# Kernel tuning notes

Measured on AMD Instinct MI355X. Metric: run time of the kernel, lower is better.

The kernel has to match this reference:

```python
import jax, jax.numpy as jnp
import numpy as np

N, F, H, E_DIM, G, NE = 20000, 128, 256, 128, 64, 320000

def _ln(x, g, b, eps=1e-5):
    m = jnp.mean(x, axis=-1, keepdims=True)
    v = jnp.mean((x - m) ** 2, axis=-1, keepdims=True)
    return (x - m) * jax.lax.rsqrt(v + eps) * g + b

def _gcn(x, src, dst, W, b, n):
    # GCNConv: h = D^{-1/2}(A+I)D^{-1/2} (x W) + b, degrees from A+I
    h = x @ W
    loop = jnp.arange(n)
    s = jnp.concatenate([src, loop])
    d = jnp.concatenate([dst, loop])
    deg = jax.ops.segment_sum(jnp.ones_like(s, dtype=h.dtype), d, num_segments=n)
    dinv = jax.lax.rsqrt(jnp.maximum(deg, 1.0))
    w_e = dinv[s] * dinv[d]  # [E+N]
    out = jax.ops.segment_sum(h[s] * w_e[:, None], d, num_segments=n)
    return out + b

def setup_inputs() -> dict:
    key = jax.random.key(0)
    ks = jax.random.split(key, 32)
    def nrm(k, shp, scale=0.05):
        return jax.random.normal(k, shp, dtype=jnp.float32) * scale
    inp = {
        'x': jax.random.normal(ks[0], (N, F), dtype=jnp.float32),
        'edge_index': jax.random.randint(ks[1], (2, NE), 0, N),
        'batch': jnp.sort(jax.random.randint(ks[2], (N,), 0, G)),
        'enc_w': nrm(ks[3], (F, H)), 'enc_b': jnp.zeros((H,), jnp.float32),
        'enc_g': jnp.ones((H,), jnp.float32), 'enc_be': jnp.zeros((H,), jnp.float32),
        'w1': nrm(ks[4], (H, H)), 'b1': jnp.zeros((H,), jnp.float32),
        'g1': jnp.ones((H,), jnp.float32), 'be1': jnp.zeros((H,), jnp.float32),
        'w2': nrm(ks[5], (H, H)), 'b2': jnp.zeros((H,), jnp.float32),
        'g2': jnp.ones((H,), jnp.float32), 'be2': jnp.zeros((H,), jnp.float32),
        'w3': nrm(ks[6], (H, H)), 'b3': jnp.zeros((H,), jnp.float32),
        'g3': jnp.ones((H,), jnp.float32), 'be3': jnp.zeros((H,), jnp.float32),
        'attn_w': nrm(ks[7], (H, 1)), 'attn_b': jnp.zeros((1,), jnp.float32),
        'pw1': nrm(ks[8], (H, H)), 'pb1': jnp.zeros((H,), jnp.float32),
        'pg': jnp.ones((H,), jnp.float32), 'pbe': jnp.zeros((H,), jnp.float32),
        'pw2': nrm(ks[9], (H, E_DIM)), 'pb2': jnp.zeros((E_DIM,), jnp.float32),
    }
    return inp

def reference(x, edge_index, batch, enc_w, enc_b, enc_g, enc_be,
              w1, b1, g1, be1, w2, b2, g2, be2, w3, b3, g3, be3,
              attn_w, attn_b, pw1, pb1, pg, pbe, pw2, pb2):
    src, dst = edge_index[0], edge_index[1]
    n = x.shape[0]
    # feature encoder (dropout = identity in eval)
    h = jax.nn.relu(_ln(x @ enc_w + enc_b, enc_g, enc_be))
    x1 = jax.nn.relu(_ln(_gcn(h, src, dst, w1, b1, n), g1, be1))
    x2 = jax.nn.relu(_ln(_gcn(x1, src, dst, w2, b2, n), g2, be2)) + x1
    x3 = jax.nn.relu(_ln(_gcn(x2, src, dst, w3, b3, n), g3, be3)) + x2
    # global softmax over the node dimension (dim=0), as in the original
    a = jnp.tanh(x3 @ attn_w + attn_b)       # [N,1]
    a = jax.nn.softmax(a, axis=0)
    pooled = jax.ops.segment_sum(x3 * a, batch, num_segments=G)  # [G,H]
    p = jax.nn.relu(_ln(pooled @ pw1 + pb1, pg, pbe))
    out = p @ pw2 + pb2                      # [G, E_DIM]
    nrm = jnp.maximum(jnp.linalg.norm(out, axis=1, keepdims=True), 1e-12)
    return out / nrm
```

## Files before the change

kernel.cpp:

```cpp
#include <hip/hip_runtime.h>
#include <hip/hip_bf16.h>

#define NN 20000
#define FF 128
#define HH 256
#define EDIM 128
#define GG 64
#define NEDGE 320000
#define PSUB 16
#define CSTRIDE 64

typedef __attribute__((ext_vector_type(4))) float f4;
typedef __attribute__((ext_vector_type(4))) float f32x4;
typedef __attribute__((ext_vector_type(8))) short bf16x8;
typedef __attribute__((ext_vector_type(4))) unsigned short u16x4;
typedef __attribute__((ext_vector_type(4))) int i32x4;

__device__ inline float wsum(float v) {
#pragma unroll
    for (int m = 32; m >= 1; m >>= 1) v += __shfl_xor(v, m, 64);
    return v;
}

__device__ inline unsigned short f2b(float f) {
    union { float f; unsigned u; } x; x.f = f;
    unsigned r = x.u + 0x7fffu + ((x.u >> 16) & 1u);
    return (unsigned short)(r >> 16);
}
__device__ inline float b2f(unsigned short u) {
    union { unsigned u; float f; } x; x.u = ((unsigned)u) << 16;
    return x.f;
}

__global__ void k_prep(const float* __restrict__ W0, const float* __restrict__ W1,
                       const float* __restrict__ W2, const float* __restrict__ W3,
                       unsigned short* __restrict__ T0, unsigned short* __restrict__ T1,
                       unsigned short* __restrict__ T2, unsigned short* __restrict__ T3,
                       int* __restrict__ cnt) {
    int b = blockIdx.x, tid = threadIdx.x;
    if (b < 20) {
        int t = b * 256 + tid;
        if (t < NN / 4) ((i32x4*)cnt)[t] = (i32x4){0, 0, 0, 0};
        return;
    }
    const float* W; unsigned short* T; int K, tt;
    if (b < 28)      { W = W0; T = T0; K = 128; tt = b - 20; }
    else if (b < 44) { W = W1; T = T1; K = 256; tt = b - 28; }
    else if (b < 60) { W = W2; T = T2; K = 256; tt = b - 44; }
    else             { W = W3; T = T3; K = 256; tt = b - 60; }
    int ktiles = K / 64;
    int kt = tt % ktiles, nt = tt / ktiles;
    int k0 = kt * 64, n0 = nt * 64;
    __shared__ unsigned short ldsT[64][65];
    int rn = (tid & 15) * 4, rk = tid >> 4;
#pragma unroll
    for (int i = 0; i < 4; i++) {
        int k = rk + 16 * i;
        f4 v = *(const f4*)(W + (size_t)(k0 + k) * 256 + n0 + rn);
#pragma unroll
        for (int j = 0; j < 4; j++) ldsT[rn + j][k] = f2b(v[j]);
    }
    __syncthreads();
    int wn = tid >> 2, kseg = (tid & 3) * 16;
#pragma unroll
    for (int q = 0; q < 4; q++) {
        u16x4 o = { ldsT[wn][kseg + q * 4 + 0], ldsT[wn][kseg + q * 4 + 1],
                    ldsT[wn][kseg + q * 4 + 2], ldsT[wn][kseg + q * 4 + 3] };
        *(u16x4*)(T + (size_t)(n0 + wn) * K + k0 + kseg + q * 4) = o;
    }
}

__global__ __launch_bounds__(256) void k_encg1(
        const float* __restrict__ X, const unsigned short* __restrict__ Wt,
        const unsigned short* __restrict__ Wt1,
        const float* __restrict__ eb, const float* __restrict__ gam,
        const float* __restrict__ bet, unsigned short* __restrict__ T1out, int M,
        const int* __restrict__ src, const int* __restrict__ dst,
        int* __restrict__ cnt, int* __restrict__ colv, int ne) {
    __shared__ unsigned short Wl[2 * 16 * 64 * 8];
    __shared__ unsigned short hs[64 * 256];
    int b = blockIdx.x, tid = threadIdx.x;
    if (b >= 313) {
        int e = (b - 313) * 256 + tid;
        if (e < ne) {
            int d = dst[e];
            int pos = atomicAdd(&cnt[d], 1);
            if (pos < CSTRIDE) colv[(size_t)d * CSTRIDE + pos] = src[e];
        }
        return;
    }
    int wave = tid >> 6, lane = tid & 63;
    int lmod = lane & 15, ldiv = lane >> 4;
    int mbase = b * 64 + wave * 16;
    int row = min(mbase + lmod, M - 1);
    f32x4 acc[16] = {};
#pragma unroll
    for (int h = 0; h < 2; h++) {
        __syncthreads();
        for (int c = tid; c < 2048; c += 256) {
            int l = c & 63, nf = (c >> 6) & 15, kss = c >> 10;
            int n = nf * 16 + (l & 15);
            int k = (h * 2 + kss) * 32 + (l >> 4) * 8;
            *(bf16x8*)(Wl + (size_t)c * 8) = *(const bf16x8*)(Wt + (size_t)n * 128 + k);
        }
        __syncthreads();
#pragma unroll
        for (int kss = 0; kss < 2; kss++) {
            int ks = h * 2 + kss;
            f4 xa = *(const f4*)(X + (size_t)row * 128 + ks * 32 + ldiv * 8);
            f4 xb2 = *(const f4*)(X + (size_t)row * 128 + ks * 32 + ldiv * 8 + 4);
            bf16x8 xf;
            xf[0] = (short)f2b(xa[0]); xf[1] = (short)f2b(xa[1]);
            xf[2] = (short)f2b(xa[2]); xf[3] = (short)f2b(xa[3]);
            xf[4] = (short)f2b(xb2[0]); xf[5] = (short)f2b(xb2[1]);
            xf[6] = (short)f2b(xb2[2]); xf[7] = (short)f2b(xb2[3]);
#pragma unroll
            for (int nf = 0; nf < 16; nf++) {
                bf16x8 wf = *(bf16x8*)(Wl + ((size_t)(kss * 16 + nf) * 64 + lane) * 8);
                acc[nf] = __builtin_amdgcn_mfma_f32_16x16x32_bf16(wf, xf, acc[nf], 0, 0, 0);
            }
        }
    }
    float vs = 0.f;
#pragma unroll
    for (int nf = 0; nf < 16; nf++) {
        f4 bb = *(const f4*)(eb + nf * 16 + ldiv * 4);
#pragma unroll
        for (int r = 0; r < 4; r++) { acc[nf][r] += bb[r]; vs += acc[nf][r]; }
    }
    vs += __shfl_xor(vs, 16, 64); vs += __shfl_xor(vs, 32, 64);
    float mean = vs * (1.0f / 256.0f);
    float ss = 0.f;
#pragma unroll
    for (int nf = 0; nf < 16; nf++) {
#pragma unroll
        for (int r = 0; r < 4; r++) { float d = acc[nf][r] - mean; ss += d * d; }
    }
    ss += __shfl_xor(ss, 16, 64); ss += __shfl_xor(ss, 32, 64);
    float rs = rsqrtf(ss * (1.0f / 256.0f) + 1e-5f);
    int r_loc = wave * 16 + lmod;
    int swz = (r_loc & 7) << 4;
#pragma unroll
    for (int nf = 0; nf < 16; nf++) {
        f4 gv = *(const f4*)(gam + nf * 16 + ldiv * 4);
        f4 bv = *(const f4*)(bet + nf * 16 + ldiv * 4);
        u16x4 o;
#pragma unroll
        for (int r = 0; r < 4; r++)
            o[r] = f2b(fmaxf((acc[nf][r] - mean) * rs * gv[r] + bv[r], 0.0f));
        int byte = ((nf * 32 + ldiv * 8) ^ swz);
        *(u16x4*)((char*)hs + (size_t)r_loc * 512 + byte) = o;
    }
    __syncthreads();
    f32x4 acc2[4][4] = {};
    const unsigned short* wb = Wt1 + (size_t)(wave * 64 + lmod) * 256 + ldiv * 8;
#pragma unroll
    for (int ks = 0; ks < 8; ks++) {
        bf16x8 wf[4], hf[4];
#pragma unroll
        for (int nf = 0; nf < 4; nf++)
            wf[nf] = *(const bf16x8*)(wb + (size_t)nf * 16 * 256 + ks * 32);
#pragma unroll
        for (int rg = 0; rg < 4; rg++) {
            int rr = rg * 16 + lmod;
            int byte = ((ks * 64 + ldiv * 16) ^ ((rr & 7) << 4));
            hf[rg] = *(const bf16x8*)((const char*)hs + (size_t)rr * 512 + byte);
        }
#pragma unroll
        for (int rg = 0; rg < 4; rg++) {
#pragma unroll
            for (int nf = 0; nf < 4; nf++) {
                acc2[rg][nf] = __builtin_amdgcn_mfma_f32_16x16x32_bf16(
                    wf[nf], hf[rg], acc2[rg][nf], 0, 0, 0);
            }
        }
    }
#pragma unroll
    for (int rg = 0; rg < 4; rg++) {
        int m = b * 64 + rg * 16 + lmod;
        if (m < M) {
#pragma unroll
            for (int nf = 0; nf < 4; nf++) {
                int n = wave * 64 + nf * 16 + ldiv * 4;
                u16x4 o = { f2b(acc2[rg][nf][0]), f2b(acc2[rg][nf][1]),
                            f2b(acc2[rg][nf][2]), f2b(acc2[rg][nf][3]) };
                *(u16x4*)(T1out + (size_t)m * 256 + n) = o;
            }
        }
    }
}

#define GEMM_NWG 628
template<int K>
__global__ __launch_bounds__(256) void bgemm(const unsigned short* __restrict__ Xb,
                                             const unsigned short* __restrict__ Wt,
                                             unsigned short* __restrict__ C, int M) {
    constexpr int KSTEPS = K / 32;
    __shared__ unsigned short Wl[KSTEPS * 4 * 64 * 8];
    int tid = threadIdx.x;
    int orig = blockIdx.y * 4 + blockIdx.x;
    int xcd = orig & 7, rest = orig >> 3;
    constexpr int q = GEMM_NWG >> 3, r = GEMM_NWG & 7;
    int wg = (xcd < r ? xcd * (q + 1) : r * (q + 1) + (xcd - r) * q) + rest;
    int m0 = wg >> 2;
    int n0 = (wg & 3) * 64;
    for (int c = tid; c < KSTEPS * 4 * 64; c += 256) {
        int lc = c & 63;
        int nf = (c >> 6) & 3;
        int ks = c >> 8;
        int n = n0 + nf * 16 + (lc & 15);
        int k = ks * 32 + (lc >> 4) * 8;
        bf16x8 v = *(const bf16x8*)(Wt + (size_t)n * K + k);
        *(bf16x8*)(Wl + (size_t)c * 8) = v;
    }
    __syncthreads();
    int wave = tid >> 6, lane = tid & 63;
    int lmod = lane & 15, ldiv = lane >> 4;
    int mbase = m0 * 128 + wave * 32;
    f32x4 acc[2][4] = {};
#pragma unroll
    for (int ks = 0; ks < KSTEPS; ks++) {
        int k0 = ks * 32 + ldiv * 8;
        bf16x8 xf[2], wf[4];
#pragma unroll
        for (int mf = 0; mf < 2; mf++) {
            int row = mbase + mf * 16 + lmod;
            row = min(row, M - 1);
            xf[mf] = *(const bf16x8*)(Xb + (size_t)row * K + k0);
        }
#pragma unroll
        for (int nf = 0; nf < 4; nf++) {
            wf[nf] = *(const bf16x8*)(Wl + ((size_t)(ks * 4 + nf) * 64 + lane) * 8);
        }
#pragma unroll
        for (int mf = 0; mf < 2; mf++) {
#pragma unroll
            for (int nf = 0; nf < 4; nf++) {
                acc[mf][nf] = __builtin_amdgcn_mfma_f32_16x16x32_bf16(
                    wf[nf], xf[mf], acc[mf][nf], 0, 0, 0);
            }
        }
    }
#pragma unroll
    for (int mf = 0; mf < 2; mf++) {
        int m = mbase + mf * 16 + lmod;
        if (m < M) {
#pragma unroll
            for (int nf = 0; nf < 4; nf++) {
                int n = n0 + nf * 16 + ldiv * 4;
                u16x4 o = { f2b(acc[mf][nf][0]), f2b(acc[mf][nf][1]),
                            f2b(acc[mf][nf][2]), f2b(acc[mf][nf][3]) };
                *(u16x4*)(C + (size_t)m * 256 + n) = o;
            }
        }
    }
}

__global__ void k_aggln(const unsigned short* __restrict__ T, const int* __restrict__ cnt,
                        const int* __restrict__ col,
                        const float* __restrict__ b, const float* __restrict__ gam,
                        const float* __restrict__ bet, const unsigned short* __restrict__ resid,
                        unsigned short* __restrict__ out,
                        const float* __restrict__ aw, const float* __restrict__ ab,
                        float* __restrict__ elog, int n) {
    int wid = (blockIdx.x * blockDim.x + threadIdx.x) >> 6;
    int lane = threadIdx.x & 63;
    if (wid >= n) return;
    int deg = min(cnt[wid], CSTRIDE);
    const int* cr = col + (size_t)wid * CSTRIDE;
    f4 a0 = {0.f,0.f,0.f,0.f}, a1 = {0.f,0.f,0.f,0.f};
    f4 a2 = {0.f,0.f,0.f,0.f}, a3 = {0.f,0.f,0.f,0.f};
    int e = 0;
    for (; e + 7 < deg; e += 8) {
        i32x4 cA = *(const i32x4*)(cr + e);
        i32x4 cB = *(const i32x4*)(cr + e + 4);
        u16x4 r0 = ((const u16x4*)(T + (size_t)cA[0] * HH))[lane];
        u16x4 r1 = ((const u16x4*)(T + (size_t)cA[1] * HH))[lane];
        u16x4 r2 = ((const u16x4*)(T + (size_t)cA[2] * HH))[lane];
        u16x4 r3 = ((const u16x4*)(T + (size_t)cA[3] * HH))[lane];
        u16x4 r4 = ((const u16x4*)(T + (size_t)cB[0] * HH))[lane];
        u16x4 r5 = ((const u16x4*)(T + (size_t)cB[1] * HH))[lane];
        u16x4 r6 = ((const u16x4*)(T + (size_t)cB[2] * HH))[lane];
        u16x4 r7 = ((const u16x4*)(T + (size_t)cB[3] * HH))[lane];
        float w0 = rsqrtf((float)(cnt[cA[0]] + 1));
        float w1 = rsqrtf((float)(cnt[cA[1]] + 1));
        float w2 = rsqrtf((float)(cnt[cA[2]] + 1));
        float w3 = rsqrtf((float)(cnt[cA[3]] + 1));
        float w4 = rsqrtf((float)(cnt[cB[0]] + 1));
        float w5 = rsqrtf((float)(cnt[cB[1]] + 1));
        float w6 = rsqrtf((float)(cnt[cB[2]] + 1));
        float w7 = rsqrtf((float)(cnt[cB[3]] + 1));
#pragma unroll
        for (int i = 0; i < 4; i++) {
            a0[i] = fmaf(w0, b2f(r0[i]), a0[i]);
            a1[i] = fmaf(w1, b2f(r1[i]), a1[i]);
            a2[i] = fmaf(w2, b2f(r2[i]), a2[i]);
            a3[i] = fmaf(w3, b2f(r3[i]), a3[i]);
            a0[i] = fmaf(w4, b2f(r4[i]), a0[i]);
            a1[i] = fmaf(w5, b2f(r5[i]), a1[i]);
            a2[i] = fmaf(w6, b2f(r6[i]), a2[i]);
            a3[i] = fmaf(w7, b2f(r7[i]), a3[i]);
        }
    }
    for (; e + 3 < deg; e += 4) {
        i32x4 c4 = *(const i32x4*)(cr + e);
        float w0 = rsqrtf((float)(cnt[c4[0]] + 1));
        float w1 = rsqrtf((float)(cnt[c4[1]] + 1));
        float w2 = rsqrtf((float)(cnt[c4[2]] + 1));
        float w3 = rsqrtf((float)(cnt[c4[3]] + 1));
        u16x4 r0 = ((const u16x4*)(T + (size_t)c4[0] * HH))[lane];
        u16x4 r1 = ((const u16x4*)(T + (size_t)c4[1] * HH))[lane];
        u16x4 r2 = ((const u16x4*)(T + (size_t)c4[2] * HH))[lane];
        u16x4 r3 = ((const u16x4*)(T + (size_t)c4[3] * HH))[lane];
#pragma unroll
        for (int i = 0; i < 4; i++) {
            a0[i] = fmaf(w0, b2f(r0[i]), a0[i]);
            a1[i] = fmaf(w1, b2f(r1[i]), a1[i]);
            a2[i] = fmaf(w2, b2f(r2[i]), a2[i]);
            a3[i] = fmaf(w3, b2f(r3[i]), a3[i]);
        }
    }
    for (; e < deg; e++) {
        int s0 = cr[e];
        float w0 = rsqrtf((float)(cnt[s0] + 1));
        u16x4 r0 = ((const u16x4*)(T + (size_t)s0 * HH))[lane];
#pragma unroll
        for (int i = 0; i < 4; i++) a0[i] = fmaf(w0, b2f(r0[i]), a0[i]);
    }
    float di = rsqrtf((float)(deg + 1));
    u16x4 sv = ((const u16x4*)(T + (size_t)wid * HH))[lane];
    f4 bb = ((const f4*)b)[lane];
    f4 v;
#pragma unroll
    for (int i = 0; i < 4; i++)
        v[i] = di * (a0[i] + a1[i] + a2[i] + a3[i]) + (di * di) * b2f(sv[i]) + bb[i];
    float s = wsum(v[0] + v[1] + v[2] + v[3]);
    float mean = s * (1.0f / HH);
    f4 d = v - mean;
    float ss = wsum(d[0] * d[0] + d[1] * d[1] + d[2] * d[2] + d[3] * d[3]);
    float rs = rsqrtf(ss * (1.0f / HH) + 1e-5f);
    f4 gv = ((const f4*)gam)[lane], bv = ((const f4*)bet)[lane];
    f4 o = d * rs * gv + bv;
#pragma unroll
    for (int i = 0; i < 4; i++) o[i] = fmaxf(o[i], 0.0f);
    if (resid != nullptr) {
        u16x4 rv = ((const u16x4*)(resid + (size_t)wid * HH))[lane];
#pragma unroll
        for (int i = 0; i < 4; i++) o[i] += b2f(rv[i]);
    }
    u16x4 ov;
#pragma unroll
    for (int i = 0; i < 4; i++) ov[i] = f2b(o[i]);
    ((u16x4*)(out + (size_t)wid * HH))[lane] = ov;
    if (elog != nullptr) {
        f4 wv = ((const f4*)aw)[lane];
        float dotv = wsum(b2f(ov[0]) * wv[0] + b2f(ov[1]) * wv[1] +
                          b2f(ov[2]) * wv[2] + b2f(ov[3]) * wv[3]);
        if (lane == 0) elog[wid] = expf(tanhf(dotv + ab[0]));
    }
}

__device__ inline int lbound(const int* __restrict__ arr, int n, int key) {
    int lo = 0, hi = n;
    while (lo < hi) {
        int mid = (lo + hi) >> 1;
        if (arr[mid] < key) lo = mid + 1; else hi = mid;
    }
    return lo;
}

__global__ __launch_bounds__(256) void k_pool(const unsigned short* __restrict__ x3,
                                              const float* __restrict__ elog,
                                              const int* __restrict__ batch,
                                              float* __restrict__ partial,
                                              float* __restrict__ esum, int n) {
    int g = blockIdx.y, s = blockIdx.x, j = threadIdx.x;
    __shared__ int slo, shi;
    if (j == 0) { slo = lbound(batch, n, g); shi = lbound(batch, n, g + 1); }
    __syncthreads();
    int lo = slo, hi = shi;
    float a0 = 0.f, a1 = 0.f;
    int i = lo + s;
    for (; i + PSUB < hi; i += 2 * PSUB) {
        a0 += elog[i] * b2f(x3[(size_t)i * HH + j]);
        a1 += elog[i + PSUB] * b2f(x3[(size_t)(i + PSUB) * HH + j]);
    }
    if (i < hi) a0 += elog[i] * b2f(x3[(size_t)i * HH + j]);
    partial[(size_t)(g * PSUB + s) * HH + j] = a0 + a1;
    if (j < 64) {
        float es = 0.f;
        for (int t = j; (size_t)lo + s + (size_t)t * PSUB < (size_t)hi; t += 64)
            es += elog[lo + s + t * PSUB];
        es = wsum(es);
        if (j == 0) esum[g * PSUB + s] = es;
    }
}

__global__ __launch_bounds__(256) void k_tail(
    const float* __restrict__ partial, const float* __restrict__ esum,
    const float* __restrict__ pw1, const float* __restrict__ pb1,
    const float* __restrict__ pg, const float* __restrict__ pbe,
    const float* __restrict__ pw2, const float* __restrict__ pb2,
    float* __restrict__ out) {
    __shared__ float pl[256];
    __shared__ float ps[256];
    __shared__ float red[256];
    __shared__ float os[128];
    int g = blockIdx.x, j = threadIdx.x;
    float t = esum[j] + esum[j + 256] + esum[j + 512] + esum[j + 768];
    red[j] = t;
    __syncthreads();
    for (int s = 128; s > 0; s >>= 1) {
        if (j < s) red[j] += red[j + s];
        __syncthreads();
    }
    float inv = 1.0f / red[0];
    __syncthreads();
    float acc = 0.f;
#pragma unroll
    for (int s = 0; s < PSUB; s++) acc += partial[(size_t)(g * PSUB + s) * HH + j];
    pl[j] = acc * inv;
    __syncthreads();
    float q = pb1[j];
#pragma unroll 8
    for (int k = 0; k < 256; k++) q = fmaf(pl[k], pw1[k * 256 + j], q);
    red[j] = q;
    __syncthreads();
    for (int s = 128; s > 0; s >>= 1) {
        if (j < s) red[j] += red[j + s];
        __syncthreads();
    }
    float mean = red[0] * (1.0f / 256.0f);
    __syncthreads();
    float d = q - mean;
    red[j] = d * d;
    __syncthreads();
    for (int s = 128; s > 0; s >>= 1) {
        if (j < s) red[j] += red[j + s];
        __syncthreads();
    }
    float var = red[0] * (1.0f / 256.0f);
    __syncthreads();
    float p = fmaxf(d * rsqrtf(var + 1e-5f) * pg[j] + pbe[j], 0.0f);
    ps[j] = p;
    __syncthreads();
    if (j < 128) {
        float o = pb2[j];
#pragma unroll 8
        for (int k = 0; k < 256; k++) o = fmaf(ps[k], pw2[k * 128 + j], o);
        os[j] = o;
    }
    __syncthreads();
    float val = (j < 128) ? os[j] * os[j] : 0.f;
    red[j] = val;
    __syncthreads();
    for (int s = 128; s > 0; s >>= 1) {
        if (j < s) red[j] += red[j + s];
        __syncthreads();
    }
    float nrm = fmaxf(sqrtf(red[0]), 1e-12f);
    if (j < 128) out[g * 128 + j] = os[j] / nrm;
}

extern "C" void kernel_launch(void* const* d_in, const int* in_sizes, int n_in,
                              void* d_out, int out_size, void* d_ws, size_t ws_size,
                              hipStream_t stream) {
    const float* x      = (const float*)d_in[0];
    const int*   ei     = (const int*)d_in[1];
    const int*   batch  = (const int*)d_in[2];
    const float* enc_w  = (const float*)d_in[3];
    const float* enc_b  = (const float*)d_in[4];
    const float* enc_g  = (const float*)d_in[5];
    const float* enc_be = (const float*)d_in[6];
    const float* w1 = (const float*)d_in[7],  *b1 = (const float*)d_in[8];
    const float* g1 = (const float*)d_in[9],  *be1 = (const float*)d_in[10];
    const float* w2 = (const float*)d_in[11], *b2 = (const float*)d_in[12];
    const float* g2 = (const float*)d_in[13], *be2 = (const float*)d_in[14];
    const float* w3 = (const float*)d_in[15], *b3 = (const float*)d_in[16];
    const float* g3 = (const float*)d_in[17], *be3 = (const float*)d_in[18];
    const float* attn_w = (const float*)d_in[19], *attn_b = (const float*)d_in[20];
    const float* pw1 = (const float*)d_in[21], *pb1 = (const float*)d_in[22];
    const float* pg  = (const float*)d_in[23], *pbe = (const float*)d_in[24];
    const float* pw2 = (const float*)d_in[25], *pb2 = (const float*)d_in[26];
    float* out = (float*)d_out;

    const int* src = ei;
    const int* dst = ei + NEDGE;

    unsigned short* us = (unsigned short*)d_ws;
    unsigned short* Tb = us;
    unsigned short* Pb = Tb + (size_t)NN * HH;
    unsigned short* Qb = Pb + (size_t)NN * HH;
    unsigned short* wte = Qb + (size_t)NN * HH;
    unsigned short* wt1 = wte + 256 * 128;
    unsigned short* wt2 = wt1 + 256 * 256;
    unsigned short* wt3 = wt2 + 256 * 256;
    float* fp = (float*)(wt3 + 256 * 256);
    float* elog    = fp;
    float* partial = elog + NN;
    float* esum    = partial + (size_t)GG * PSUB * HH;
    int* cnt = (int*)(esum + GG * PSUB);
    int* col = cnt + NN;

    k_prep<<<76, 256, 0, stream>>>(enc_w, w1, w2, w3, wte, wt1, wt2, wt3, cnt);
    k_encg1<<<313 + 1250, 256, 0, stream>>>(x, wte, wt1, enc_b, enc_g, enc_be, Tb, NN,
                                            src, dst, cnt, col, NEDGE);

    dim3 gg(4, 157);
    k_aggln<<<(NN + 3) / 4, 256, 0, stream>>>(Tb, cnt, col, b1, g1, be1, nullptr, Qb,
                                              nullptr, nullptr, nullptr, NN);
    bgemm<256><<<gg, 256, 0, stream>>>(Qb, wt2, Tb, NN);
    k_aggln<<<(NN + 3) / 4, 256, 0, stream>>>(Tb, cnt, col, b2, g2, be2, Qb, Pb,
                                              nullptr, nullptr, nullptr, NN);
    bgemm<256><<<gg, 256, 0, stream>>>(Pb, wt3, Tb, NN);
    k_aggln<<<(NN + 3) / 4, 256, 0, stream>>>(Tb, cnt, col, b3, g3, be3, Pb, Qb,
                                              attn_w, attn_b, elog, NN);
    k_pool<<<dim3(PSUB, GG), 256, 0, stream>>>(Qb, elog, batch, partial, esum, NN);
    k_tail<<<GG, 256, 0, stream>>>(partial, esum, pw1, pb1, pg, pbe, pw2, pb2, out);
}
```

Measured before the change: 183.1 us.

## Fuse GCN aggregation+LayerNorm with next layer's GEMM into one kernel

Replaces the separate k_aggln and bgemm launches for layers 1 and 2 with a fused kernel. Each 1024-thread block aggregates and normalizes 16 nodes, stages them in swizzled LDS, then multiplies by the next weight matrix with MFMA. This removes the round trip of the normalized activations through global memory and two kernel launches. In exchange, every block rereads the full 256x256 weight from global/L2 with no LDS reuse across blocks, and an extra ping-pong buffer is needed.

```diff
diff --git a/kernel.cpp b/kernel.cpp
--- a/kernel.cpp
+++ b/kernel.cpp
@@ -190,70 +190,119 @@
     }
 }
 
-#define GEMM_NWG 628
-template<int K>
-__global__ __launch_bounds__(256) void bgemm(const unsigned short* __restrict__ Xb,
-                                             const unsigned short* __restrict__ Wt,
-                                             unsigned short* __restrict__ C, int M) {
-    constexpr int KSTEPS = K / 32;
-    __shared__ unsigned short Wl[KSTEPS * 4 * 64 * 8];
+__global__ __launch_bounds__(1024) void k_agg_gemm(
+        const unsigned short* __restrict__ T, const int* __restrict__ cnt,
+        const int* __restrict__ col,
+        const float* __restrict__ b, const float* __restrict__ gam,
+        const float* __restrict__ bet, const unsigned short* __restrict__ resid,
+        unsigned short* __restrict__ x_out,
+        const unsigned short* __restrict__ Wtn, unsigned short* __restrict__ Tnext,
+        int n) {
+    __shared__ unsigned short hs[16 * 256];
     int tid = threadIdx.x;
-    int orig = blockIdx.y * 4 + blockIdx.x;
-    int xcd = orig & 7, rest = orig >> 3;
-    constexpr int q = GEMM_NWG >> 3, r = GEMM_NWG & 7;
-    int wg = (xcd < r ? xcd * (q + 1) : r * (q + 1) + (xcd - r) * q) + rest;
-    int m0 = wg >> 2;
-    int n0 = (wg & 3) * 64;
-    for (int c = tid; c < KSTEPS * 4 * 64; c += 256) {
-        int lc = c & 63;
-        int nf = (c >> 6) & 3;
-        int ks = c >> 8;
-        int n = n0 + nf * 16 + (lc & 15);
-        int k = ks * 32 + (lc >> 4) * 8;
-        bf16x8 v = *(const bf16x8*)(Wt + (size_t)n * K + k);
-        *(bf16x8*)(Wl + (size_t)c * 8) = v;
-    }
-    __syncthreads();
     int wave = tid >> 6, lane = tid & 63;
+    int wid = blockIdx.x * 16 + wave;
+    int deg = min(cnt[wid], CSTRIDE);
+    const int* cr = col + (size_t)wid * CSTRIDE;
+    f4 a0 = {0.f,0.f,0.f,0.f}, a1 = {0.f,0.f,0.f,0.f};
+    f4 a2 = {0.f,0.f,0.f,0.f}, a3 = {0.f,0.f,0.f,0.f};
+    int e = 0;
+    for (; e + 7 < deg; e += 8) {
+        i32x4 cA = *(const i32x4*)(cr + e);
+        i32x4 cB = *(const i32x4*)(cr + e + 4);
+        u16x4 r0 = ((const u16x4*)(T + (size_t)cA[0] * HH))[lane];
+        u16x4 r1 = ((const u16x4*)(T + (size_t)cA[1] * HH))[lane];
+        u16x4 r2 = ((const u16x4*)(T + (size_t)cA[2] * HH))[lane];
+        u16x4 r3 = ((const u16x4*)(T + (size_t)cA[3] * HH))[lane];
+        u16x4 r4 = ((const u16x4*)(T + (size_t)cB[0] * HH))[lane];
+        u16x4 r5 = ((const u16x4*)(T + (size_t)cB[1] * HH))[lane];
+        u16x4 r6 = ((const u16x4*)(T + (size_t)cB[2] * HH))[lane];
+        u16x4 r7 = ((const u16x4*)(T + (size_t)cB[3] * HH))[lane];
+        float w0 = rsqrtf((float)(cnt[cA[0]] + 1));
+        float w1 = rsqrtf((float)(cnt[cA[1]] + 1));
+        float w2 = rsqrtf((float)(cnt[cA[2]] + 1));
+        float w3 = rsqrtf((float)(cnt[cA[3]] + 1));
+        float w4 = rsqrtf((float)(cnt[cB[0]] + 1));
+        float w5 = rsqrtf((float)(cnt[cB[1]] + 1));
+        float w6 = rsqrtf((float)(cnt[cB[2]] + 1));
+        float w7 = rsqrtf((float)(cnt[cB[3]] + 1));
+#pragma unroll
+        for (int i = 0; i < 4; i++) {
+            a0[i] = fmaf(w0, b2f(r0[i]), a0[i]);
+            a1[i] = fmaf(w1, b2f(r1[i]), a1[i]);
+            a2[i] = fmaf(w2, b2f(r2[i]), a2[i]);
+            a3[i] = fmaf(w3, b2f(r3[i]), a3[i]);
+            a0[i] = fmaf(w4, b2f(r4[i]), a0[i]);
+            a1[i] = fmaf(w5, b2f(r5[i]), a1[i]);
+            a2[i] = fmaf(w6, b2f(r6[i]), a2[i]);
+            a3[i] = fmaf(w7, b2f(r7[i]), a3[i]);
+        }
+    }
+    for (; e + 3 < deg; e += 4) {
+        i32x4 c4 = *(const i32x4*)(cr + e);
+        float w0 = rsqrtf((float)(cnt[c4[0]] + 1));
+        float w1 = rsqrtf((float)(cnt[c4[1]] + 1));
+        float w2 = rsqrtf((float)(cnt[c4[2]] + 1));
+        float w3 = rsqrtf((float)(cnt[c4[3]] + 1));
+        u16x4 r0 = ((const u16x4*)(T + (size_t)c4[0] * HH))[lane];
+        u16x4 r1 = ((const u16x4*)(T + (size_t)c4[1] * HH))[lane];
+        u16x4 r2 = ((const u16x4*)(T + (size_t)c4[2] * HH))[lane];
+        u16x4 r3 = ((const u16x4*)(T + (size_t)c4[3] * HH))[lane];
+#pragma unroll
+        for (int i = 0; i < 4; i++) {
+            a0[i] = fmaf(w0, b2f(r0[i]), a0[i]);
+            a1[i] = fmaf(w1, b2f(r1[i]), a1[i]);
+            a2[i] = fmaf(w2, b2f(r2[i]), a2[i]);
+            a3[i] = fmaf(w3, b2f(r3[i]), a3[i]);
+        }
+    }
+    for (; e < deg; e++) {
+        int s0 = cr[e];
+        float w0 = rsqrtf((float)(cnt[s0] + 1));
+        u16x4 r0 = ((const u16x4*)(T + (size_t)s0 * HH))[lane];
+#pragma unroll
+        for (int i = 0; i < 4; i++) a0[i] = fmaf(w0, b2f(r0[i]), a0[i]);
+    }
+    float di = rsqrtf((float)(deg + 1));
+    u16x4 sv = ((const u16x4*)(T + (size_t)wid * HH))[lane];
+    f4 bb = ((const f4*)b)[lane];
+    f4 v;
+#pragma unroll
+    for (int i = 0; i < 4; i++)
+        v[i] = di * (a0[i] + a1[i] + a2[i] + a3[i]) + (di * di) * b2f(sv[i]) + bb[i];
+    float s = wsum(v[0] + v[1] + v[2] + v[3]);
+    float mean = s * (1.0f / HH);
+    f4 d = v - mean;
+    float ss = wsum(d[0] * d[0] + d[1] * d[1] + d[2] * d[2] + d[3] * d[3]);
+    float rs = rsqrtf(ss * (1.0f / HH) + 1e-5f);
+    f4 gv = ((const f4*)gam)[lane], bv = ((const f4*)bet)[lane];
+    f4 o = d * rs * gv + bv;
+#pragma unroll
+    for (int i = 0; i < 4; i++) o[i] = fmaxf(o[i], 0.0f);
+    if (resid != nullptr) {
+        u16x4 rv = ((const u16x4*)(resid + (size_t)wid * HH))[lane];
+#pragma unroll
+        for (int i = 0; i < 4; i++) o[i] += b2f(rv[i]);
+    }
+    u16x4 ov;
+#pragma unroll
+    for (int i = 0; i < 4; i++) ov[i] = f2b(o[i]);
+    ((u16x4*)(x_out + (size_t)wid * HH))[lane] = ov;
+    *(u16x4*)((char*)hs + (size_t)wave * 512 + ((lane * 8) ^ ((wave & 7) << 4))) = ov;
+    __syncthreads();
     int lmod = lane & 15, ldiv = lane >> 4;
-    int mbase = m0 * 128 + wave * 32;
-    f32x4 acc[2][4] = {};
-#pragma unroll
-    for (int ks = 0; ks < KSTEPS; ks++) {
-        int k0 = ks * 32 + ldiv * 8;
-        bf16x8 xf[2], wf[4];
-#pragma unroll
-        for (int mf = 0; mf < 2; mf++) {
-            int row = mbase + mf * 16 + lmod;
-            row = min(row, M - 1);
-            xf[mf] = *(const bf16x8*)(Xb + (size_t)row * K + k0);
-        }
-#pragma unroll
-        for (int nf = 0; nf < 4; nf++) {
-            wf[nf] = *(const bf16x8*)(Wl + ((size_t)(ks * 4 + nf) * 64 + lane) * 8);
-        }
-#pragma unroll
-        for (int mf = 0; mf < 2; mf++) {
-#pragma unroll
-            for (int nf = 0; nf < 4; nf++) {
-                acc[mf][nf] = __builtin_amdgcn_mfma_f32_16x16x32_bf16(
-                    wf[nf], xf[mf], acc[mf][nf], 0, 0, 0);
-            }
-        }
-    }
-#pragma unroll
-    for (int mf = 0; mf < 2; mf++) {
-        int m = mbase + mf * 16 + lmod;
-        if (m < M) {
-#pragma unroll
-            for (int nf = 0; nf < 4; nf++) {
-                int n = n0 + nf * 16 + ldiv * 4;
-                u16x4 o = { f2b(acc[mf][nf][0]), f2b(acc[mf][nf][1]),
-                            f2b(acc[mf][nf][2]), f2b(acc[mf][nf][3]) };
-                *(u16x4*)(C + (size_t)m * 256 + n) = o;
-            }
-        }
-    }
+    f32x4 acc2 = {};
+    const unsigned short* wb = Wtn + (size_t)(wave * 16 + lmod) * 256 + ldiv * 8;
+#pragma unroll
+    for (int ks = 0; ks < 8; ks++) {
+        bf16x8 wf = *(const bf16x8*)(wb + ks * 32);
+        int byte = ((ks * 64 + ldiv * 16) ^ ((lmod & 7) << 4));
+        bf16x8 hf = *(const bf16x8*)((const char*)hs + (size_t)lmod * 512 + byte);
+        acc2 = __builtin_amdgcn_mfma_f32_16x16x32_bf16(wf, hf, acc2, 0, 0, 0);
+    }
+    int m = blockIdx.x * 16 + lmod;
+    u16x4 oo = { f2b(acc2[0]), f2b(acc2[1]), f2b(acc2[2]), f2b(acc2[3]) };
+    *(u16x4*)(Tnext + (size_t)m * 256 + wave * 16 + ldiv * 4) = oo;
 }
 
 __global__ void k_aggln(const unsigned short* __restrict__ T, const int* __restrict__ cnt,
@@ -491,7 +540,8 @@
     unsigned short* Tb = us;
     unsigned short* Pb = Tb + (size_t)NN * HH;
     unsigned short* Qb = Pb + (size_t)NN * HH;
-    unsigned short* wte = Qb + (size_t)NN * HH;
+    unsigned short* Ub = Qb + (size_t)NN * HH;
+    unsigned short* wte = Ub + (size_t)NN * HH;
     unsigned short* wt1 = wte + 256 * 128;
     unsigned short* wt2 = wt1 + 256 * 256;
     unsigned short* wt3 = wt2 + 256 * 256;
@@ -505,14 +555,10 @@
     k_prep<<<76, 256, 0, stream>>>(enc_w, w1, w2, w3, wte, wt1, wt2, wt3, cnt);
     k_encg1<<<313 + 1250, 256, 0, stream>>>(x, wte, wt1, enc_b, enc_g, enc_be, Tb, NN,
                                             src, dst, cnt, col, NEDGE);
-
-    dim3 gg(4, 157);
-    k_aggln<<<(NN + 3) / 4, 256, 0, stream>>>(Tb, cnt, col, b1, g1, be1, nullptr, Qb,
-                                              nullptr, nullptr, nullptr, NN);
-    bgemm<256><<<gg, 256, 0, stream>>>(Qb, wt2, Tb, NN);
-    k_aggln<<<(NN + 3) / 4, 256, 0, stream>>>(Tb, cnt, col, b2, g2, be2, Qb, Pb,
-                                              nullptr, nullptr, nullptr, NN);
-    bgemm<256><<<gg, 256, 0, stream>>>(Pb, wt3, Tb, NN);
+    k_agg_gemm<<<NN / 16, 1024, 0, stream>>>(Tb, cnt, col, b1, g1, be1, nullptr,
+                                             Qb, wt2, Ub, NN);
+    k_agg_gemm<<<NN / 16, 1024, 0, stream>>>(Ub, cnt, col, b2, g2, be2, Qb,
+                                             Pb, wt3, Tb, NN);
     k_aggln<<<(NN + 3) / 4, 256, 0, stream>>>(Tb, cnt, col, b3, g3, be3, Pb, Qb,
                                               attn_w, attn_b, elog, NN);
     k_pool<<<dim3(PSUB, GG), 256, 0, stream>>>(Qb, elog, batch, partial, esum, NN);
```

Measured after the change: 206.3 us. 1.13x slower.
